# Kernel optimization log

Measured on AMD Instinct MI355X. Metric: run time of the kernel, lower is better.

## Reference

```python
import jax, jax.numpy as jnp
import numpy as np

ALPHA = 0.02
NEG = -9e15

def lrelu(x):
    return jnp.where(x >= 0, x, ALPHA * x)

def layer_norm(x, eps=1e-5):
    m = jnp.mean(x, axis=-1, keepdims=True)
    v = jnp.var(x, axis=-1, keepdims=True)
    return (x - m) * jax.lax.rsqrt(v + eps)

def setup_inputs() -> dict:
    key = jax.random.key(0)
    ks = jax.random.split(key, 10)
    B, N, F_IN, D = 8, 2048, 10, 128
    h = jax.random.normal(ks[0], (B, N, F_IN), jnp.float32)
    adj = jax.random.randint(ks[1], (B, N, N), 0, 2, jnp.int32)
    s = 0.1
    return {
        "h": h,
        "adj": adj,
        "W1": jax.random.normal(ks[2], (D, F_IN), jnp.float32) * s,
        "b1": jax.random.normal(ks[3], (D,), jnp.float32) * s,
        "Wg": jax.random.normal(ks[4], (D, D), jnp.float32) * s,
        "bg": jax.random.normal(ks[5], (D,), jnp.float32) * s,
        "a1": jax.random.normal(ks[6], (D,), jnp.float32) * s,
        "a2": jax.random.normal(ks[7], (D,), jnp.float32) * s,
        "W2": jax.random.normal(ks[8], (2, D), jnp.float32) * s,
        "b2": jax.random.normal(ks[9], (2,), jnp.float32) * s,
    }

def reference(h, adj, W1, b1, Wg, bg, a1, a2, W2, b2):
    # fc1 + layernorm + leakyrelu
    x = h @ W1.T + b1                      # [B,N,128]
    x = lrelu(layer_norm(x))
    # GAT layer
    Wh = x @ Wg.T + bg                     # [B,N,128]
    e1 = Wh @ a1                           # [B,N]
    e2 = Wh @ a2                           # [B,N]
    e = lrelu(e1[:, :, None] + e2[:, None, :])  # [B,N,N]
    e = jnp.where(adj != 0, e, NEG)
    attn = jax.nn.softmax(e, axis=2)
    hp = jnp.einsum('bij,bjd->bid', attn, Wh)    # [B,N,128]
    hp = lrelu(layer_norm(hp))
    # global max pool over nodes
    pooled = jnp.max(hp, axis=1)           # [B,128]
    out = pooled @ W2.T + b2               # [B,2]
    return jax.nn.log_softmax(out, axis=-1)
```

## Files before the change

### kernel.cpp

```cpp
#include <hip/hip_runtime.h>

#define B 8
#define N 2048
#define FIN 10
#define D 128
#define ALPHA 0.02f
#define LOG2E 1.44269504088896340736f
#define BR 32
#define TI 32
#define JC 128
#define NBLK_ATTN ((N / TI) * B)

typedef short bf8 __attribute__((ext_vector_type(8)));
typedef short s4v __attribute__((ext_vector_type(4)));
typedef float f32x4 __attribute__((ext_vector_type(4)));

__device__ __forceinline__ float lrelu(float x) { return x >= 0.f ? x : ALPHA * x; }

__device__ __forceinline__ short f2b(float f) {
    unsigned u = __float_as_uint(f);
    return (short)((u + 0x7fffu + ((u >> 16) & 1u)) >> 16);
}

__device__ __forceinline__ float fexp2(float x) {
#if __has_builtin(__builtin_amdgcn_exp2f)
    return __builtin_amdgcn_exp2f(x);
#else
    return exp2f(x);
#endif
}

__device__ __forceinline__ unsigned pack2(float lo, float hi) {
#if __has_builtin(__builtin_amdgcn_perm)
    return __builtin_amdgcn_perm(__float_as_uint(hi), __float_as_uint(lo), 0x07060302u);
#else
    return (__float_as_uint(hi) & 0xFFFF0000u) | (__float_as_uint(lo) >> 16);
#endif
}

__device__ __forceinline__ unsigned enc_key(float v) {
    unsigned b = __float_as_uint(v);
    return (b & 0x80000000u) ? ~b : (b | 0x80000000u);
}
__device__ __forceinline__ float dec_key(unsigned k) {
    unsigned b = (k & 0x80000000u) ? (k & 0x7fffffffu) : ~k;
    return __uint_as_float(b);
}

__global__ __launch_bounds__(256) void k_prep(
    const float* __restrict__ Wg, unsigned short* __restrict__ Wgb,
    unsigned* __restrict__ pooled, unsigned* __restrict__ cnt)
{
    const int g = blockIdx.x * 256 + threadIdx.x;
    float4 f = *(const float4*)&Wg[g * 4];
    s4v v;
    v[0] = f2b(f.x); v[1] = f2b(f.y); v[2] = f2b(f.z); v[3] = f2b(f.w);
    *(s4v*)&Wgb[g * 4] = v;
    if (g < B * D) pooled[g] = 0u;
    if (g == B * D) *cnt = 0u;
}

__global__ __launch_bounds__(256) void k_proj(
    const float* __restrict__ h, const float* __restrict__ W1, const float* __restrict__ b1,
    const unsigned short* __restrict__ Wgb, const float* __restrict__ bg,
    const float* __restrict__ a1, const float* __restrict__ a2,
    unsigned short* __restrict__ WhT, float* __restrict__ e1g, float* __restrict__ e2g)
{
    __shared__ __align__(16) short xep_lds[32 * 136];
    __shared__ __align__(16) short wg_lds[D * 136];
    __shared__ float W1_lds[D * 11];
    __shared__ float h_lds[BR * FIN];
    __shared__ float ep1[2][BR], ep2[2][BR];

    const int t = threadIdx.x;
    const int r0 = blockIdx.x * BR;
    const int bb = r0 >> 11;
    const int jloc = r0 & (N - 1);

    for (int idx = t; idx < D * FIN; idx += 256)
        W1_lds[(idx / FIN) * 11 + (idx % FIN)] = W1[idx];
    for (int idx = t; idx < BR * FIN; idx += 256)
        h_lds[idx] = h[(size_t)r0 * FIN + idx];
    __syncthreads();

    {
        const int dr = t >> 4;
        const int j8 = t & 15;
        #pragma unroll
        for (int pass = 0; pass < 8; pass++) {
            int dd = pass * 16 + dr;
            *(bf8*)&wg_lds[dd * 136 + j8 * 8] = *(const bf8*)&Wgb[dd * D + j8 * 8];
        }
    }

    const int w = t >> 6, lane = t & 63;
    {
        float b1v0 = b1[lane], b1v1 = b1[lane + 64];
        for (int i = 0; i < 8; i++) {
            int r = w * 8 + i;
            float s0 = b1v0, s1 = b1v1;
            const float* hr = &h_lds[r * FIN];
            #pragma unroll
            for (int k = 0; k < FIN; k++) {
                float hv = hr[k];
                s0 += hv * W1_lds[lane * 11 + k];
                s1 += hv * W1_lds[(lane + 64) * 11 + k];
            }
            float sm = s0 + s1, sq = s0 * s0 + s1 * s1;
            #pragma unroll
            for (int m = 1; m <= 32; m <<= 1) { sm += __shfl_xor(sm, m); sq += __shfl_xor(sq, m); }
            float mean = sm * (1.f / D);
            float var  = sq * (1.f / D) - mean * mean;
            float rs = rsqrtf(var + 1e-5f);
            xep_lds[r * 136 + lane]      = f2b(lrelu((s0 - mean) * rs));
            xep_lds[r * 136 + lane + 64] = f2b(lrelu((s1 - mean) * rs));
        }
    }
    __syncthreads();

    const int l15 = lane & 15, q = lane >> 4;
    const int mw = w & 1, np = w >> 1;
    f32x4 acc[4];
    #pragma unroll
    for (int nt = 0; nt < 4; nt++)
        #pragma unroll
        for (int r = 0; r < 4; r++) acc[nt][r] = 0.f;

    #pragma unroll
    for (int ks = 0; ks < 4; ks++) {
        bf8 av = *(const bf8*)&xep_lds[(mw * 16 + l15) * 136 + ks * 32 + q * 8];
        #pragma unroll
        for (int nt = 0; nt < 4; nt++) {
            bf8 bv = *(const bf8*)&wg_lds[((np * 4 + nt) * 16 + l15) * 136 + ks * 32 + q * 8];
            acc[nt] = __builtin_amdgcn_mfma_f32_16x16x32_bf16(av, bv, acc[nt], 0, 0, 0);
        }
    }

    float e1p[4] = {0.f, 0.f, 0.f, 0.f}, e2p[4] = {0.f, 0.f, 0.f, 0.f};
    #pragma unroll
    for (int nt = 0; nt < 4; nt++) {
        int col = (np * 4 + nt) * 16 + l15;
        float bgv = bg[col], a1v = a1[col], a2v = a2[col];
        #pragma unroll
        for (int r = 0; r < 4; r++) {
            float v = acc[nt][r] + bgv;
            acc[nt][r] = v;
            e1p[r] += v * a1v;
            e2p[r] += v * a2v;
        }
    }
    #pragma unroll
    for (int m = 1; m <= 8; m <<= 1) {
        #pragma unroll
        for (int r = 0; r < 4; r++) { e1p[r] += __shfl_xor(e1p[r], m); e2p[r] += __shfl_xor(e2p[r], m); }
    }
    if (l15 == 0) {
        #pragma unroll
        for (int r = 0; r < 4; r++) {
            ep1[np][mw * 16 + q * 4 + r] = e1p[r];
            ep2[np][mw * 16 + q * 4 + r] = e2p[r];
        }
    }
    __syncthreads();
    if (t < BR) {
        e1g[r0 + t] = (ep1[0][t] + ep1[1][t]) * LOG2E;
        e2g[r0 + t] = (ep2[0][t] + ep2[1][t]) * LOG2E;
    }
    #pragma unroll
    for (int nt = 0; nt < 4; nt++) {
        int col = (np * 4 + nt) * 16 + l15;
        #pragma unroll
        for (int r = 0; r < 4; r++)
            xep_lds[col * 36 + mw * 16 + q * 4 + r] = f2b(acc[nt][r]);
    }
    __syncthreads();
    {
        const int col = t >> 1, jh = (t & 1) * 16;
        unsigned short* dst = WhT + ((size_t)(bb * D + col)) * N + jloc + jh;
        #pragma unroll
        for (int i2 = 0; i2 < 4; i2++)
            *(uint2*)(dst + i2 * 4) = *(const uint2*)&xep_lds[col * 36 + jh + i2 * 4];
    }
}

__global__ __launch_bounds__(512) void k_attn(
    const int* __restrict__ adj, const unsigned short* __restrict__ WhT,
    const float* __restrict__ e1g, const float* __restrict__ e2g,
    unsigned* __restrict__ pooled, unsigned* __restrict__ cnt,
    const float* __restrict__ W2, const float* __restrict__ b2,
    float* __restrict__ out)
{
    __shared__ __align__(16) short pT[TI * 136];
    __shared__ __align__(16) short whT[D * 136];
    __shared__ float statsp[4][TI][2];
    __shared__ float maxb[2][D];
    __shared__ int finalflag;

    const int t = threadIdx.x;
    const int b = blockIdx.y;
    const int i0 = blockIdx.x * TI;

    const int w = t >> 6, lane = t & 63;
    const int l15 = lane & 15, q = lane >> 4;
    const int mw = w & 1;
    const int np = w >> 1;

    const int rg = t >> 5;
    const int jq = (t & 31) * 4;
    const int dr = t >> 4;
    const int j8 = t & 15;

    const float e1r0 = e1g[b * N + i0 + rg * 2];
    const float e1r1 = e1g[b * N + i0 + rg * 2 + 1];

    const unsigned short* WhTb = WhT + (size_t)b * D * N;
    const int* adjb = adj + ((size_t)b * N + i0) * N;

    f32x4 acc[2], accl;
    #pragma unroll
    for (int nt = 0; nt < 2; nt++)
        #pragma unroll
        for (int r = 0; r < 4; r++) acc[nt][r] = 0.f;
    #pragma unroll
    for (int r = 0; r < 4; r++) accl[r] = 0.f;

    bf8 ones;
    #pragma unroll
    for (int i = 0; i < 8; i++) ones[i] = (short)0x3F80;

    int4 a0 = *(const int4*)(adjb + (size_t)(rg * 2) * N + jq);
    int4 a1r = *(const int4*)(adjb + (size_t)(rg * 2 + 1) * N + jq);
    float4 e2r = *(const float4*)&e2g[b * N + jq];
    bf8 wr0 = *(const bf8*)(WhTb + (size_t)(0 * 32 + dr) * N + j8 * 8);
    bf8 wr1 = *(const bf8*)(WhTb + (size_t)(1 * 32 + dr) * N + j8 * 8);
    bf8 wr2 = *(const bf8*)(WhTb + (size_t)(2 * 32 + dr) * N + j8 * 8);
    bf8 wr3 = *(const bf8*)(WhTb + (size_t)(3 * 32 + dr) * N + j8 * 8);

    for (int jc = 0; jc < N / JC; jc++) {
        {
            float s0 = e1r0 + e2r.x, s1 = e1r0 + e2r.y,
                  s2 = e1r0 + e2r.z, s3 = e1r0 + e2r.w;
            float p0 = a0.x ? fexp2(fmaxf(s0, ALPHA * s0)) : 0.f;
            float p1 = a0.y ? fexp2(fmaxf(s1, ALPHA * s1)) : 0.f;
            float p2 = a0.z ? fexp2(fmaxf(s2, ALPHA * s2)) : 0.f;
            float p3 = a0.w ? fexp2(fmaxf(s3, ALPHA * s3)) : 0.f;
            *(uint2*)&pT[(rg * 2) * 136 + jq] = make_uint2(pack2(p0, p1), pack2(p2, p3));

            s0 = e1r1 + e2r.x; s1 = e1r1 + e2r.y;
            s2 = e1r1 + e2r.z; s3 = e1r1 + e2r.w;
            p0 = a1r.x ? fexp2(fmaxf(s0, ALPHA * s0)) : 0.f;
            p1 = a1r.y ? fexp2(fmaxf(s1, ALPHA * s1)) : 0.f;
            p2 = a1r.z ? fexp2(fmaxf(s2, ALPHA * s2)) : 0.f;
            p3 = a1r.w ? fexp2(fmaxf(s3, ALPHA * s3)) : 0.f;
            *(uint2*)&pT[(rg * 2 + 1) * 136 + jq] = make_uint2(pack2(p0, p1), pack2(p2, p3));

            *(bf8*)&whT[(0 * 32 + dr) * 136 + j8 * 8] = wr0;
            *(bf8*)&whT[(1 * 32 + dr) * 136 + j8 * 8] = wr1;
            *(bf8*)&whT[(2 * 32 + dr) * 136 + j8 * 8] = wr2;
            *(bf8*)&whT[(3 * 32 + dr) * 136 + j8 * 8] = wr3;
        }
        __syncthreads();

        if (jc < N / JC - 1) {
            const int j0n = (jc + 1) * JC;
            a0  = *(const int4*)(adjb + (size_t)(rg * 2) * N + j0n + jq);
            a1r = *(const int4*)(adjb + (size_t)(rg * 2 + 1) * N + j0n + jq);
            e2r = *(const float4*)&e2g[b * N + j0n + jq];
            wr0 = *(const bf8*)(WhTb + (size_t)(0 * 32 + dr) * N + j0n + j8 * 8);
            wr1 = *(const bf8*)(WhTb + (size_t)(1 * 32 + dr) * N + j0n + j8 * 8);
            wr2 = *(const bf8*)(WhTb + (size_t)(2 * 32 + dr) * N + j0n + j8 * 8);
            wr3 = *(const bf8*)(WhTb + (size_t)(3 * 32 + dr) * N + j0n + j8 * 8);
        }

        #pragma unroll
        for (int ks = 0; ks < 4; ks++) {
            bf8 av = *(const bf8*)&pT[(mw * 16 + l15) * 136 + ks * 32 + q * 8];
            #pragma unroll
            for (int nt = 0; nt < 2; nt++) {
                bf8 bv = *(const bf8*)&whT[((np * 2 + nt) * 16 + l15) * 136 + ks * 32 + q * 8];
                acc[nt] = __builtin_amdgcn_mfma_f32_16x16x32_bf16(av, bv, acc[nt], 0, 0, 0);
            }
            accl = __builtin_amdgcn_mfma_f32_16x16x32_bf16(av, ones, accl, 0, 0, 0);
        }
        __syncthreads();
    }

    float smr[4] = {0.f, 0.f, 0.f, 0.f}, sqr[4] = {0.f, 0.f, 0.f, 0.f};
    #pragma unroll
    for (int r = 0; r < 4; r++) {
        float rinv = 1.f / accl[r];
        #pragma unroll
        for (int nt = 0; nt < 2; nt++) {
            float v = acc[nt][r] * rinv;
            acc[nt][r] = v;
            smr[r] += v;
            sqr[r] += v * v;
        }
    }
    #pragma unroll
    for (int m = 1; m <= 8; m <<= 1) {
        #pragma unroll
        for (int r = 0; r < 4; r++) { smr[r] += __shfl_xor(smr[r], m); sqr[r] += __shfl_xor(sqr[r], m); }
    }
    if (l15 == 0) {
        #pragma unroll
        for (int r = 0; r < 4; r++) {
            statsp[np][mw * 16 + q * 4 + r][0] = smr[r];
            statsp[np][mw * 16 + q * 4 + r][1] = sqr[r];
        }
    }
    __syncthreads();

    float mx[2] = {-1e30f, -1e30f};
    #pragma unroll
    for (int r = 0; r < 4; r++) {
        int row = mw * 16 + q * 4 + r;
        float s0 = statsp[0][row][0] + statsp[1][row][0] + statsp[2][row][0] + statsp[3][row][0];
        float s1 = statsp[0][row][1] + statsp[1][row][1] + statsp[2][row][1] + statsp[3][row][1];
        float mean = s0 * (1.f / D);
        float var  = s1 * (1.f / D) - mean * mean;
        float rs = rsqrtf(var + 1e-5f);
        #pragma unroll
        for (int nt = 0; nt < 2; nt++) {
            float v = lrelu((acc[nt][r] - mean) * rs);
            mx[nt] = fmaxf(mx[nt], v);
        }
    }
    #pragma unroll
    for (int m = 16; m <= 32; m <<= 1) {
        #pragma unroll
        for (int nt = 0; nt < 2; nt++) mx[nt] = fmaxf(mx[nt], __shfl_xor(mx[nt], m));
    }
    if (q == 0) {
        #pragma unroll
        for (int nt = 0; nt < 2; nt++) maxb[mw][(np * 2 + nt) * 16 + l15] = mx[nt];
    }
    __syncthreads();
    if (t < D) {
        float v = fmaxf(maxb[0][t], maxb[1][t]);
        atomicMax(&pooled[b * D + t], enc_key(v));
    }
    __syncthreads();

    if (t == 0) {
        __threadfence();
        unsigned old = atomicAdd(cnt, 1u);
        finalflag = (old == NBLK_ATTN - 1) ? 1 : 0;
    }
    __syncthreads();
    if (finalflag && t < 256) {
        const int fb = t >> 5;
        const int fq = t & 31;
        float s0 = 0.f, s1 = 0.f;
        #pragma unroll
        for (int m = 0; m < 4; m++) {
            int dd = fq + 32 * m;
            unsigned key = __hip_atomic_load(&pooled[fb * D + dd], __ATOMIC_RELAXED,
                                             __HIP_MEMORY_SCOPE_AGENT);
            float v = dec_key(key);
            s0 += v * W2[dd];
            s1 += v * W2[D + dd];
        }
        #pragma unroll
        for (int m = 1; m <= 16; m <<= 1) { s0 += __shfl_xor(s0, m); s1 += __shfl_xor(s1, m); }
        if (fq == 0) {
            float o0 = s0 + b2[0], o1 = s1 + b2[1];
            float mxv = fmaxf(o0, o1);
            float ls = logf(__expf(o0 - mxv) + __expf(o1 - mxv));
            out[fb * 2 + 0] = o0 - mxv - ls;
            out[fb * 2 + 1] = o1 - mxv - ls;
        }
    }
}

extern "C" void kernel_launch(void* const* d_in, const int* in_sizes, int n_in,
                              void* d_out, int out_size, void* d_ws, size_t ws_size,
                              hipStream_t stream) {
    const float* h   = (const float*)d_in[0];
    const int*   adj = (const int*)d_in[1];
    const float* W1  = (const float*)d_in[2];
    const float* b1  = (const float*)d_in[3];
    const float* Wg  = (const float*)d_in[4];
    const float* bg  = (const float*)d_in[5];
    const float* a1  = (const float*)d_in[6];
    const float* a2  = (const float*)d_in[7];
    const float* W2  = (const float*)d_in[8];
    const float* b2  = (const float*)d_in[9];
    float* out = (float*)d_out;

    unsigned short* WhT = (unsigned short*)d_ws;
    float* e1g = (float*)((char*)d_ws + (size_t)B * D * N * 2);
    float* e2g = e1g + (size_t)B * N;
    unsigned* pooled = (unsigned*)(e2g + (size_t)B * N);
    unsigned* cnt = pooled + (size_t)B * D;
    unsigned short* Wgb = (unsigned short*)(cnt + 4);

    k_prep<<<16, 256, 0, stream>>>(Wg, Wgb, pooled, cnt);
    k_proj<<<(B * N) / BR, 256, 0, stream>>>(h, W1, b1, Wgb, bg, a1, a2,
                                             WhT, e1g, e2g);
    k_attn<<<dim3(N / TI, B), 512, 0, stream>>>(adj, WhT, e1g, e2g, pooled, cnt,
                                                W2, b2, out);
}
```

Before: 239.7 us.

## Restructure attention kernel to per-wave register-direct MFMA without LDS staging

The attention kernel is rewritten so each wave owns a 16-row tile and loads adjacency, e2 and WhT fragments straight from global memory into MFMA operand registers, double-buffered in two register stages. This removes the LDS staging of P and WhT and the two block barriers per chunk, and lets each wave compute layernorm stats without cross-wave LDS reduction. The trade-off is that WhT is no longer shared through LDS, so each wave re-reads it from global/L2, and register pressure rises with 8 accumulators and two stages. Separately, the proj kernel batches its 8 rows of shuffle reductions for more ILP.

Measured after the change: 274.8 us. 1.15x slower.

```diff
diff --git a/kernel.cpp b/kernel.cpp
--- a/kernel.cpp
+++ b/kernel.cpp
@@ -7,13 +7,12 @@
 #define ALPHA 0.02f
 #define LOG2E 1.44269504088896340736f
 #define BR 32
-#define TI 32
-#define JC 128
-#define NBLK_ATTN ((N / TI) * B)
+#define NBLK_ATTN 256
 
 typedef short bf8 __attribute__((ext_vector_type(8)));
 typedef short s4v __attribute__((ext_vector_type(4)));
 typedef float f32x4 __attribute__((ext_vector_type(4)));
+typedef unsigned u4v __attribute__((ext_vector_type(4)));
 
 __device__ __forceinline__ float lrelu(float x) { return x >= 0.f ? x : ALPHA * x; }
 
@@ -96,24 +95,33 @@
     const int w = t >> 6, lane = t & 63;
     {
         float b1v0 = b1[lane], b1v1 = b1[lane + 64];
+        float sA[8], sB[8], smv[8], sqv[8];
+        #pragma unroll
         for (int i = 0; i < 8; i++) {
-            int r = w * 8 + i;
+            const float* hr = &h_lds[(w * 8 + i) * FIN];
             float s0 = b1v0, s1 = b1v1;
-            const float* hr = &h_lds[r * FIN];
             #pragma unroll
             for (int k = 0; k < FIN; k++) {
                 float hv = hr[k];
                 s0 += hv * W1_lds[lane * 11 + k];
                 s1 += hv * W1_lds[(lane + 64) * 11 + k];
             }
-            float sm = s0 + s1, sq = s0 * s0 + s1 * s1;
+            sA[i] = s0; sB[i] = s1;
+            smv[i] = s0 + s1; sqv[i] = s0 * s0 + s1 * s1;
+        }
+        #pragma unroll
+        for (int m = 1; m <= 32; m <<= 1) {
             #pragma unroll
-            for (int m = 1; m <= 32; m <<= 1) { sm += __shfl_xor(sm, m); sq += __shfl_xor(sq, m); }
-            float mean = sm * (1.f / D);
-            float var  = sq * (1.f / D) - mean * mean;
+            for (int i = 0; i < 8; i++) { smv[i] += __shfl_xor(smv[i], m); sqv[i] += __shfl_xor(sqv[i], m); }
+        }
+        #pragma unroll
+        for (int i = 0; i < 8; i++) {
+            int r = w * 8 + i;
+            float mean = smv[i] * (1.f / D);
+            float var  = sqv[i] * (1.f / D) - mean * mean;
             float rs = rsqrtf(var + 1e-5f);
-            xep_lds[r * 136 + lane]      = f2b(lrelu((s0 - mean) * rs));
-            xep_lds[r * 136 + lane + 64] = f2b(lrelu((s1 - mean) * rs));
+            xep_lds[r * 136 + lane]      = f2b(lrelu((sA[i] - mean) * rs));
+            xep_lds[r * 136 + lane + 64] = f2b(lrelu((sB[i] - mean) * rs));
         }
     }
     __syncthreads();
@@ -183,42 +191,73 @@
     }
 }
 
-__global__ __launch_bounds__(512) void k_attn(
+struct Stage {
+    int4 a0, a1;
+    float4 e20, e21;
+    bf8 wv[8];
+};
+
+__device__ __forceinline__ void load_stage(Stage& s, const int* adjp,
+        const float* e2p, const unsigned short* whp, int c) {
+    const int off = c * 32;
+    s.a0  = *(const int4*)(adjp + off);
+    s.a1  = *(const int4*)(adjp + off + 4);
+    s.e20 = *(const float4*)(e2p + off);
+    s.e21 = *(const float4*)(e2p + off + 4);
+    #pragma unroll
+    for (int nt = 0; nt < 8; nt++)
+        s.wv[nt] = *(const bf8*)(whp + (size_t)nt * 16 * N + off);
+}
+
+__device__ __forceinline__ void consume(const Stage& s, float e1v,
+        f32x4* acc, f32x4& accl, bf8 ones) {
+    float t0 = e1v + s.e20.x, t1 = e1v + s.e20.y, t2 = e1v + s.e20.z, t3 = e1v + s.e20.w;
+    float t4 = e1v + s.e21.x, t5 = e1v + s.e21.y, t6 = e1v + s.e21.z, t7 = e1v + s.e21.w;
+    float p0 = s.a0.x ? fexp2(fmaxf(t0, ALPHA * t0)) : 0.f;
+    float p1 = s.a0.y ? fexp2(fmaxf(t1, ALPHA * t1)) : 0.f;
+    float p2 = s.a0.z ? fexp2(fmaxf(t2, ALPHA * t2)) : 0.f;
+    float p3 = s.a0.w ? fexp2(fmaxf(t3, ALPHA * t3)) : 0.f;
+    float p4 = s.a1.x ? fexp2(fmaxf(t4, ALPHA * t4)) : 0.f;
+    float p5 = s.a1.y ? fexp2(fmaxf(t5, ALPHA * t5)) : 0.f;
+    float p6 = s.a1.z ? fexp2(fmaxf(t6, ALPHA * t6)) : 0.f;
+    float p7 = s.a1.w ? fexp2(fmaxf(t7, ALPHA * t7)) : 0.f;
+    u4v uu;
+    uu.x = pack2(p0, p1); uu.y = pack2(p2, p3);
+    uu.z = pack2(p4, p5); uu.w = pack2(p6, p7);
+    bf8 av = *(bf8*)&uu;
+    #pragma unroll
+    for (int nt = 0; nt < 8; nt++)
+        acc[nt] = __builtin_amdgcn_mfma_f32_16x16x32_bf16(av, s.wv[nt], acc[nt], 0, 0, 0);
+    accl = __builtin_amdgcn_mfma_f32_16x16x32_bf16(av, ones, accl, 0, 0, 0);
+}
+
+__global__ __launch_bounds__(256) void k_attn(
     const int* __restrict__ adj, const unsigned short* __restrict__ WhT,
     const float* __restrict__ e1g, const float* __restrict__ e2g,
     unsigned* __restrict__ pooled, unsigned* __restrict__ cnt,
     const float* __restrict__ W2, const float* __restrict__ b2,
     float* __restrict__ out)
 {
-    __shared__ __align__(16) short pT[TI * 136];
-    __shared__ __align__(16) short whT[D * 136];
-    __shared__ float statsp[4][TI][2];
-    __shared__ float maxb[2][D];
+    __shared__ unsigned maxb[4][D];
     __shared__ int finalflag;
 
     const int t = threadIdx.x;
-    const int b = blockIdx.y;
-    const int i0 = blockIdx.x * TI;
-
     const int w = t >> 6, lane = t & 63;
     const int l15 = lane & 15, q = lane >> 4;
-    const int mw = w & 1;
-    const int np = w >> 1;
-
-    const int rg = t >> 5;
-    const int jq = (t & 31) * 4;
-    const int dr = t >> 4;
-    const int j8 = t & 15;
-
-    const float e1r0 = e1g[b * N + i0 + rg * 2];
-    const float e1r1 = e1g[b * N + i0 + rg * 2 + 1];
-
-    const unsigned short* WhTb = WhT + (size_t)b * D * N;
-    const int* adjb = adj + ((size_t)b * N + i0) * N;
-
-    f32x4 acc[2], accl;
-    #pragma unroll
-    for (int nt = 0; nt < 2; nt++)
+    const int bid = blockIdx.x;
+    const int b = bid >> 5;
+    const int tile = (bid & 31) * 4 + w;
+    const int i0 = tile * 16;
+
+    const float e1v = e1g[b * N + i0 + l15];
+
+    const int* adjp = adj + ((size_t)b * N + i0 + l15) * N + q * 8;
+    const float* e2p = e2g + b * N + q * 8;
+    const unsigned short* whp = WhT + (size_t)b * D * N + (size_t)l15 * N + q * 8;
+
+    f32x4 acc[8], accl;
+    #pragma unroll
+    for (int nt = 0; nt < 8; nt++)
         #pragma unroll
         for (int r = 0; r < 4; r++) acc[nt][r] = 0.f;
     #pragma unroll
@@ -228,100 +267,45 @@
     #pragma unroll
     for (int i = 0; i < 8; i++) ones[i] = (short)0x3F80;
 
-    int4 a0 = *(const int4*)(adjb + (size_t)(rg * 2) * N + jq);
-    int4 a1r = *(const int4*)(adjb + (size_t)(rg * 2 + 1) * N + jq);
-    float4 e2r = *(const float4*)&e2g[b * N + jq];
-    bf8 wr0 = *(const bf8*)(WhTb + (size_t)(0 * 32 + dr) * N + j8 * 8);
-    bf8 wr1 = *(const bf8*)(WhTb + (size_t)(1 * 32 + dr) * N + j8 * 8);
-    bf8 wr2 = *(const bf8*)(WhTb + (size_t)(2 * 32 + dr) * N + j8 * 8);
-    bf8 wr3 = *(const bf8*)(WhTb + (size_t)(3 * 32 + dr) * N + j8 * 8);
-
-    for (int jc = 0; jc < N / JC; jc++) {
-        {
-            float s0 = e1r0 + e2r.x, s1 = e1r0 + e2r.y,
-                  s2 = e1r0 + e2r.z, s3 = e1r0 + e2r.w;
-            float p0 = a0.x ? fexp2(fmaxf(s0, ALPHA * s0)) : 0.f;
-            float p1 = a0.y ? fexp2(fmaxf(s1, ALPHA * s1)) : 0.f;
-            float p2 = a0.z ? fexp2(fmaxf(s2, ALPHA * s2)) : 0.f;
-            float p3 = a0.w ? fexp2(fmaxf(s3, ALPHA * s3)) : 0.f;
-            *(uint2*)&pT[(rg * 2) * 136 + jq] = make_uint2(pack2(p0, p1), pack2(p2, p3));
-
-            s0 = e1r1 + e2r.x; s1 = e1r1 + e2r.y;
-            s2 = e1r1 + e2r.z; s3 = e1r1 + e2r.w;
-            p0 = a1r.x ? fexp2(fmaxf(s0, ALPHA * s0)) : 0.f;
-            p1 = a1r.y ? fexp2(fmaxf(s1, ALPHA * s1)) : 0.f;
-            p2 = a1r.z ? fexp2(fmaxf(s2, ALPHA * s2)) : 0.f;
-            p3 = a1r.w ? fexp2(fmaxf(s3, ALPHA * s3)) : 0.f;
-            *(uint2*)&pT[(rg * 2 + 1) * 136 + jq] = make_uint2(pack2(p0, p1), pack2(p2, p3));
-
-            *(bf8*)&whT[(0 * 32 + dr) * 136 + j8 * 8] = wr0;
-            *(bf8*)&whT[(1 * 32 + dr) * 136 + j8 * 8] = wr1;
-            *(bf8*)&whT[(2 * 32 + dr) * 136 + j8 * 8] = wr2;
-            *(bf8*)&whT[(3 * 32 + dr) * 136 + j8 * 8] = wr3;
-        }
-        __syncthreads();
-
-        if (jc < N / JC - 1) {
-            const int j0n = (jc + 1) * JC;
-            a0  = *(const int4*)(adjb + (size_t)(rg * 2) * N + j0n + jq);
-            a1r = *(const int4*)(adjb + (size_t)(rg * 2 + 1) * N + j0n + jq);
-            e2r = *(const float4*)&e2g[b * N + j0n + jq];
-            wr0 = *(const bf8*)(WhTb + (size_t)(0 * 32 + dr) * N + j0n + j8 * 8);
-            wr1 = *(const bf8*)(WhTb + (size_t)(1 * 32 + dr) * N + j0n + j8 * 8);
-            wr2 = *(const bf8*)(WhTb + (size_t)(2 * 32 + dr) * N + j0n + j8 * 8);
-            wr3 = *(const bf8*)(WhTb + (size_t)(3 * 32 + dr) * N + j0n + j8 * 8);
-        }
-
-        #pragma unroll
-        for (int ks = 0; ks < 4; ks++) {
-            bf8 av = *(const bf8*)&pT[(mw * 16 + l15) * 136 + ks * 32 + q * 8];
-            #pragma unroll
-            for (int nt = 0; nt < 2; nt++) {
-                bf8 bv = *(const bf8*)&whT[((np * 2 + nt) * 16 + l15) * 136 + ks * 32 + q * 8];
-                acc[nt] = __builtin_amdgcn_mfma_f32_16x16x32_bf16(av, bv, acc[nt], 0, 0, 0);
-            }
-            accl = __builtin_amdgcn_mfma_f32_16x16x32_bf16(av, ones, accl, 0, 0, 0);
-        }
-        __syncthreads();
-    }
-
-    float smr[4] = {0.f, 0.f, 0.f, 0.f}, sqr[4] = {0.f, 0.f, 0.f, 0.f};
+    Stage SA, SB;
+    load_stage(SA, adjp, e2p, whp, 0);
+    load_stage(SB, adjp, e2p, whp, 1);
+
+    for (int c = 0; c < N / 32; c += 2) {
+        consume(SA, e1v, acc, accl, ones);
+        if (c + 2 < N / 32) load_stage(SA, adjp, e2p, whp, c + 2);
+        consume(SB, e1v, acc, accl, ones);
+        if (c + 3 < N / 32) load_stage(SB, adjp, e2p, whp, c + 3);
+    }
+
+    float smr[4], sqr[4];
     #pragma unroll
     for (int r = 0; r < 4; r++) {
         float rinv = 1.f / accl[r];
-        #pragma unroll
-        for (int nt = 0; nt < 2; nt++) {
+        float sm = 0.f, sq = 0.f;
+        #pragma unroll
+        for (int nt = 0; nt < 8; nt++) {
             float v = acc[nt][r] * rinv;
             acc[nt][r] = v;
-            smr[r] += v;
-            sqr[r] += v * v;
-        }
+            sm += v; sq += v * v;
+        }
+        smr[r] = sm; sqr[r] = sq;
     }
     #pragma unroll
     for (int m = 1; m <= 8; m <<= 1) {
         #pragma unroll
         for (int r = 0; r < 4; r++) { smr[r] += __shfl_xor(smr[r], m); sqr[r] += __shfl_xor(sqr[r], m); }
     }
-    if (l15 == 0) {
-        #pragma unroll
-        for (int r = 0; r < 4; r++) {
-            statsp[np][mw * 16 + q * 4 + r][0] = smr[r];
-            statsp[np][mw * 16 + q * 4 + r][1] = sqr[r];
-        }
-    }
-    __syncthreads();
-
-    float mx[2] = {-1e30f, -1e30f};
+    float mx[8];
+    #pragma unroll
+    for (int nt = 0; nt < 8; nt++) mx[nt] = -1e30f;
     #pragma unroll
     for (int r = 0; r < 4; r++) {
-        int row = mw * 16 + q * 4 + r;
-        float s0 = statsp[0][row][0] + statsp[1][row][0] + statsp[2][row][0] + statsp[3][row][0];
-        float s1 = statsp[0][row][1] + statsp[1][row][1] + statsp[2][row][1] + statsp[3][row][1];
-        float mean = s0 * (1.f / D);
-        float var  = s1 * (1.f / D) - mean * mean;
+        float mean = smr[r] * (1.f / D);
+        float var  = sqr[r] * (1.f / D) - mean * mean;
         float rs = rsqrtf(var + 1e-5f);
         #pragma unroll
-        for (int nt = 0; nt < 2; nt++) {
+        for (int nt = 0; nt < 8; nt++) {
             float v = lrelu((acc[nt][r] - mean) * rs);
             mx[nt] = fmaxf(mx[nt], v);
         }
@@ -329,16 +313,17 @@
     #pragma unroll
     for (int m = 16; m <= 32; m <<= 1) {
         #pragma unroll
-        for (int nt = 0; nt < 2; nt++) mx[nt] = fmaxf(mx[nt], __shfl_xor(mx[nt], m));
-    }
-    if (q == 0) {
-        #pragma unroll
-        for (int nt = 0; nt < 2; nt++) maxb[mw][(np * 2 + nt) * 16 + l15] = mx[nt];
+        for (int nt = 0; nt < 8; nt++) mx[nt] = fmaxf(mx[nt], __shfl_xor(mx[nt], m));
+    }
+    if (lane < 16) {
+        #pragma unroll
+        for (int nt = 0; nt < 8; nt++) maxb[w][nt * 16 + lane] = enc_key(mx[nt]);
     }
     __syncthreads();
     if (t < D) {
-        float v = fmaxf(maxb[0][t], maxb[1][t]);
-        atomicMax(&pooled[b * D + t], enc_key(v));
+        unsigned m01 = maxb[0][t] > maxb[1][t] ? maxb[0][t] : maxb[1][t];
+        unsigned m23 = maxb[2][t] > maxb[3][t] ? maxb[2][t] : maxb[3][t];
+        atomicMax(&pooled[b * D + t], m01 > m23 ? m01 : m23);
     }
     __syncthreads();
 
@@ -348,7 +333,7 @@
         finalflag = (old == NBLK_ATTN - 1) ? 1 : 0;
     }
     __syncthreads();
-    if (finalflag && t < 256) {
+    if (finalflag) {
         const int fb = t >> 5;
         const int fq = t & 31;
         float s0 = 0.f, s1 = 0.f;
@@ -398,6 +383,6 @@
     k_prep<<<16, 256, 0, stream>>>(Wg, Wgb, pooled, cnt);
     k_proj<<<(B * N) / BR, 256, 0, stream>>>(h, W1, b1, Wgb, bg, a1, a2,
                                              WhT, e1g, e2g);
-    k_attn<<<dim3(N / TI, B), 512, 0, stream>>>(adj, WhT, e1g, e2g, pooled, cnt,
-                                                W2, b2, out);
-}
+    k_attn<<<NBLK_ATTN, 256, 0, stream>>>(adj, WhT, e1g, e2g, pooled, cnt,
+                                          W2, b2, out);
+}
```

## Double-buffer register prefetch in attention loop and batch layernorm shuffles

Applied to the files above, without the earlier changes.

The attention kernel now keeps two register stages of adjacency, e2 and WhT data and prefetches two chunks ahead instead of one, to hide more global-load latency behind the MFMA phase. It also adds a min-blocks hint (launch_bounds 512,4), which caps register use. The fc1 layernorm batches eight rows' cross-lane shuffle reductions together to expose instruction-level parallelism. The extra stage raises register pressure, and the occupancy hint could force spills.

After: 243.5 us. About the same (+1.6%).

```diff
diff --git a/kernel.cpp b/kernel.cpp
--- a/kernel.cpp
+++ b/kernel.cpp
@@ -96,24 +96,33 @@
     const int w = t >> 6, lane = t & 63;
     {
         float b1v0 = b1[lane], b1v1 = b1[lane + 64];
+        float sA[8], sB[8], smv[8], sqv[8];
+        #pragma unroll
         for (int i = 0; i < 8; i++) {
-            int r = w * 8 + i;
+            const float* hr = &h_lds[(w * 8 + i) * FIN];
             float s0 = b1v0, s1 = b1v1;
-            const float* hr = &h_lds[r * FIN];
             #pragma unroll
             for (int k = 0; k < FIN; k++) {
                 float hv = hr[k];
                 s0 += hv * W1_lds[lane * 11 + k];
                 s1 += hv * W1_lds[(lane + 64) * 11 + k];
             }
-            float sm = s0 + s1, sq = s0 * s0 + s1 * s1;
+            sA[i] = s0; sB[i] = s1;
+            smv[i] = s0 + s1; sqv[i] = s0 * s0 + s1 * s1;
+        }
+        #pragma unroll
+        for (int m = 1; m <= 32; m <<= 1) {
             #pragma unroll
-            for (int m = 1; m <= 32; m <<= 1) { sm += __shfl_xor(sm, m); sq += __shfl_xor(sq, m); }
-            float mean = sm * (1.f / D);
-            float var  = sq * (1.f / D) - mean * mean;
+            for (int i = 0; i < 8; i++) { smv[i] += __shfl_xor(smv[i], m); sqv[i] += __shfl_xor(sqv[i], m); }
+        }
+        #pragma unroll
+        for (int i = 0; i < 8; i++) {
+            int r = w * 8 + i;
+            float mean = smv[i] * (1.f / D);
+            float var  = sqv[i] * (1.f / D) - mean * mean;
             float rs = rsqrtf(var + 1e-5f);
-            xep_lds[r * 136 + lane]      = f2b(lrelu((s0 - mean) * rs));
-            xep_lds[r * 136 + lane + 64] = f2b(lrelu((s1 - mean) * rs));
+            xep_lds[r * 136 + lane]      = f2b(lrelu((sA[i] - mean) * rs));
+            xep_lds[r * 136 + lane + 64] = f2b(lrelu((sB[i] - mean) * rs));
         }
     }
     __syncthreads();
@@ -183,7 +192,48 @@
     }
 }
 
-__global__ __launch_bounds__(512) void k_attn(
+struct Stage {
+    int4 a0, a1;
+    float4 e2r;
+    bf8 wr[4];
+};
+
+__device__ __forceinline__ void load_stage(Stage& s,
+        const int* adjp0, const int* adjp1, const float* e2p,
+        const unsigned short* whp, int j0) {
+    s.a0  = *(const int4*)(adjp0 + j0);
+    s.a1  = *(const int4*)(adjp1 + j0);
+    s.e2r = *(const float4*)(e2p + j0);
+    #pragma unroll
+    for (int p = 0; p < 4; p++)
+        s.wr[p] = *(const bf8*)(whp + (size_t)p * 32 * N + j0);
+}
+
+__device__ __forceinline__ void stage_to_lds(const Stage& s,
+        float e1r0, float e1r1, short* pT, short* whT,
+        int rg, int jq, int dr, int j8) {
+    float t0 = e1r0 + s.e2r.x, t1 = e1r0 + s.e2r.y,
+          t2 = e1r0 + s.e2r.z, t3 = e1r0 + s.e2r.w;
+    float p0 = s.a0.x ? fexp2(fmaxf(t0, ALPHA * t0)) : 0.f;
+    float p1 = s.a0.y ? fexp2(fmaxf(t1, ALPHA * t1)) : 0.f;
+    float p2 = s.a0.z ? fexp2(fmaxf(t2, ALPHA * t2)) : 0.f;
+    float p3 = s.a0.w ? fexp2(fmaxf(t3, ALPHA * t3)) : 0.f;
+    *(uint2*)&pT[(rg * 2) * 136 + jq] = make_uint2(pack2(p0, p1), pack2(p2, p3));
+
+    t0 = e1r1 + s.e2r.x; t1 = e1r1 + s.e2r.y;
+    t2 = e1r1 + s.e2r.z; t3 = e1r1 + s.e2r.w;
+    p0 = s.a1.x ? fexp2(fmaxf(t0, ALPHA * t0)) : 0.f;
+    p1 = s.a1.y ? fexp2(fmaxf(t1, ALPHA * t1)) : 0.f;
+    p2 = s.a1.z ? fexp2(fmaxf(t2, ALPHA * t2)) : 0.f;
+    p3 = s.a1.w ? fexp2(fmaxf(t3, ALPHA * t3)) : 0.f;
+    *(uint2*)&pT[(rg * 2 + 1) * 136 + jq] = make_uint2(pack2(p0, p1), pack2(p2, p3));
+
+    #pragma unroll
+    for (int p = 0; p < 4; p++)
+        *(bf8*)&whT[(p * 32 + dr) * 136 + j8 * 8] = s.wr[p];
+}
+
+__global__ __launch_bounds__(512, 4) void k_attn(
     const int* __restrict__ adj, const unsigned short* __restrict__ WhT,
     const float* __restrict__ e1g, const float* __restrict__ e2g,
     unsigned* __restrict__ pooled, unsigned* __restrict__ cnt,
@@ -214,7 +264,10 @@
     const float e1r1 = e1g[b * N + i0 + rg * 2 + 1];
 
     const unsigned short* WhTb = WhT + (size_t)b * D * N;
-    const int* adjb = adj + ((size_t)b * N + i0) * N;
+    const int* adjp0 = adj + ((size_t)b * N + i0 + rg * 2) * N + jq;
+    const int* adjp1 = adjp0 + N;
+    const float* e2p = e2g + b * N + jq;
+    const unsigned short* whp = WhTb + (size_t)dr * N + j8 * 8;
 
     f32x4 acc[2], accl;
     #pragma unroll
@@ -228,62 +281,36 @@
     #pragma unroll
     for (int i = 0; i < 8; i++) ones[i] = (short)0x3F80;
 
-    int4 a0 = *(const int4*)(adjb + (size_t)(rg * 2) * N + jq);
-    int4 a1r = *(const int4*)(adjb + (size_t)(rg * 2 + 1) * N + jq);
-    float4 e2r = *(const float4*)&e2g[b * N + jq];
-    bf8 wr0 = *(const bf8*)(WhTb + (size_t)(0 * 32 + dr) * N + j8 * 8);
-    bf8 wr1 = *(const bf8*)(WhTb + (size_t)(1 * 32 + dr) * N + j8 * 8);
-    bf8 wr2 = *(const bf8*)(WhTb + (size_t)(2 * 32 + dr) * N + j8 * 8);
-    bf8 wr3 = *(const bf8*)(WhTb + (size_t)(3 * 32 + dr) * N + j8 * 8);
-
-    for (int jc = 0; jc < N / JC; jc++) {
-        {
-            float s0 = e1r0 + e2r.x, s1 = e1r0 + e2r.y,
-                  s2 = e1r0 + e2r.z, s3 = e1r0 + e2r.w;
-            float p0 = a0.x ? fexp2(fmaxf(s0, ALPHA * s0)) : 0.f;
-            float p1 = a0.y ? fexp2(fmaxf(s1, ALPHA * s1)) : 0.f;
-            float p2 = a0.z ? fexp2(fmaxf(s2, ALPHA * s2)) : 0.f;
-            float p3 = a0.w ? fexp2(fmaxf(s3, ALPHA * s3)) : 0.f;
-            *(uint2*)&pT[(rg * 2) * 136 + jq] = make_uint2(pack2(p0, p1), pack2(p2, p3));
-
-            s0 = e1r1 + e2r.x; s1 = e1r1 + e2r.y;
-            s2 = e1r1 + e2r.z; s3 = e1r1 + e2r.w;
-            p0 = a1r.x ? fexp2(fmaxf(s0, ALPHA * s0)) : 0.f;
-            p1 = a1r.y ? fexp2(fmaxf(s1, ALPHA * s1)) : 0.f;
-            p2 = a1r.z ? fexp2(fmaxf(s2, ALPHA * s2)) : 0.f;
-            p3 = a1r.w ? fexp2(fmaxf(s3, ALPHA * s3)) : 0.f;
-            *(uint2*)&pT[(rg * 2 + 1) * 136 + jq] = make_uint2(pack2(p0, p1), pack2(p2, p3));
-
-            *(bf8*)&whT[(0 * 32 + dr) * 136 + j8 * 8] = wr0;
-            *(bf8*)&whT[(1 * 32 + dr) * 136 + j8 * 8] = wr1;
-            *(bf8*)&whT[(2 * 32 + dr) * 136 + j8 * 8] = wr2;
-            *(bf8*)&whT[(3 * 32 + dr) * 136 + j8 * 8] = wr3;
-        }
+    Stage S0, S1;
+    load_stage(S0, adjp0, adjp1, e2p, whp, 0);
+    load_stage(S1, adjp0, adjp1, e2p, whp, JC);
+
+    #define MFMA_PHASE() do {                                                        \
+        _Pragma("unroll")                                                            \
+        for (int ks = 0; ks < 4; ks++) {                                             \
+            bf8 av = *(const bf8*)&pT[(mw * 16 + l15) * 136 + ks * 32 + q * 8];      \
+            _Pragma("unroll")                                                        \
+            for (int nt = 0; nt < 2; nt++) {                                         \
+                bf8 bv = *(const bf8*)&whT[((np * 2 + nt) * 16 + l15) * 136 + ks * 32 + q * 8]; \
+                acc[nt] = __builtin_amdgcn_mfma_f32_16x16x32_bf16(av, bv, acc[nt], 0, 0, 0);    \
+            }                                                                        \
+            accl = __builtin_amdgcn_mfma_f32_16x16x32_bf16(av, ones, accl, 0, 0, 0); \
+        }                                                                            \
+    } while (0)
+
+    for (int c = 0; c < N / JC; c += 2) {
+        stage_to_lds(S0, e1r0, e1r1, pT, whT, rg, jq, dr, j8);
         __syncthreads();
-
-        if (jc < N / JC - 1) {
-            const int j0n = (jc + 1) * JC;
-            a0  = *(const int4*)(adjb + (size_t)(rg * 2) * N + j0n + jq);
-            a1r = *(const int4*)(adjb + (size_t)(rg * 2 + 1) * N + j0n + jq);
-            e2r = *(const float4*)&e2g[b * N + j0n + jq];
-            wr0 = *(const bf8*)(WhTb + (size_t)(0 * 32 + dr) * N + j0n + j8 * 8);
-            wr1 = *(const bf8*)(WhTb + (size_t)(1 * 32 + dr) * N + j0n + j8 * 8);
-            wr2 = *(const bf8*)(WhTb + (size_t)(2 * 32 + dr) * N + j0n + j8 * 8);
-            wr3 = *(const bf8*)(WhTb + (size_t)(3 * 32 + dr) * N + j0n + j8 * 8);
-        }
-
-        #pragma unroll
-        for (int ks = 0; ks < 4; ks++) {
-            bf8 av = *(const bf8*)&pT[(mw * 16 + l15) * 136 + ks * 32 + q * 8];
-            #pragma unroll
-            for (int nt = 0; nt < 2; nt++) {
-                bf8 bv = *(const bf8*)&whT[((np * 2 + nt) * 16 + l15) * 136 + ks * 32 + q * 8];
-                acc[nt] = __builtin_amdgcn_mfma_f32_16x16x32_bf16(av, bv, acc[nt], 0, 0, 0);
-            }
-            accl = __builtin_amdgcn_mfma_f32_16x16x32_bf16(av, ones, accl, 0, 0, 0);
-        }
+        if (c + 2 < N / JC) load_stage(S0, adjp0, adjp1, e2p, whp, (c + 2) * JC);
+        MFMA_PHASE();
         __syncthreads();
-    }
+        stage_to_lds(S1, e1r0, e1r1, pT, whT, rg, jq, dr, j8);
+        __syncthreads();
+        if (c + 3 < N / JC) load_stage(S1, adjp0, adjp1, e2p, whp, (c + 3) * JC);
+        MFMA_PHASE();
+        __syncthreads();
+    }
+    #undef MFMA_PHASE
 
     float smr[4] = {0.f, 0.f, 0.f, 0.f}, sqr[4] = {0.f, 0.f, 0.f, 0.f};
     #pragma unroll
```
